# Kernel tuning notes

Measured on AMD Instinct MI355X. Metric: run time of the kernel, lower is better.

The kernel has to match this reference:

```python
import jax, jax.numpy as jnp
import numpy as np

D_MODEL = 1024
NUM_HEADS = 16
HEAD_DIM = D_MODEL // NUM_HEADS
B, S = 2, 2048


def setup_inputs() -> dict:
    key = jax.random.key(0)
    ks = jax.random.split(key, 6)
    scale = 0.02
    return {
        "x": jax.random.normal(ks[0], (B, S, D_MODEL), dtype=jnp.float32),
        "mask": jax.random.normal(ks[1], (S, S), dtype=jnp.float32),
        "Wqkv": jax.random.normal(ks[2], (D_MODEL, 3 * D_MODEL), dtype=jnp.float32) * scale,
        "bqkv": jax.random.normal(ks[3], (3 * D_MODEL,), dtype=jnp.float32) * scale,
        "Wout": jax.random.normal(ks[4], (D_MODEL, D_MODEL), dtype=jnp.float32) * scale,
        "bout": jax.random.normal(ks[5], (D_MODEL,), dtype=jnp.float32) * scale,
    }


def reference(x, mask, Wqkv, bqkv, Wout, bout):
    b, s, d = x.shape
    h, hd = NUM_HEADS, HEAD_DIM
    qkv = x @ Wqkv + bqkv                              # [b, s, 3d]
    qkv = qkv.reshape(b, s, h, 3 * hd).transpose(0, 2, 1, 3)  # [b, h, s, 3hd]
    q, k, v = jnp.split(qkv, 3, axis=-1)               # each [b, h, s, hd]
    scaled = jnp.einsum("bhqd,bhkd->bhqk", q, k) / jnp.sqrt(jnp.float32(hd))
    scaled = scaled + mask                             # mask [s, s] broadcasts
    attn = jax.nn.softmax(scaled, axis=-1)
    values = jnp.einsum("bhqk,bhkd->bhqd", attn, v)    # [b, h, s, hd]
    values = values.transpose(0, 2, 1, 3).reshape(b, s, d)
    return values @ Wout + bout
```

## Files before the change

### kernel.cpp

```cpp
#include <hip/hip_runtime.h>
#include <hip/hip_bf16.h>

#define D_MODEL 1024
#define NH 16
#define HD 64
#define BATCH 2
#define SEQ 2048
#define M_TOTAL (BATCH*SEQ)

typedef _Float16 f16;
typedef _Float16 half8 __attribute__((ext_vector_type(8)));
typedef _Float16 half4v __attribute__((ext_vector_type(4)));
typedef float floatx4 __attribute__((ext_vector_type(4)));

__device__ inline void gload_lds16(const void* g, void* l) {
    __builtin_amdgcn_global_load_lds(
        (const __attribute__((address_space(1))) unsigned int*)g,
        (__attribute__((address_space(3))) unsigned int*)l, 16, 0, 0);
}

__global__ void cvt_f32_f16(const float* __restrict__ src, f16* __restrict__ dst, int n4) {
    int i = blockIdx.x * blockDim.x + threadIdx.x;
    if (i < n4) {
        float4 v = ((const float4*)src)[i];
        half4v o = { (f16)v.x, (f16)v.y, (f16)v.z, (f16)v.w };
        *(half4v*)(dst + (long)i * 4) = o;
    }
}

__global__ void transpose_cvt(const float* __restrict__ src, f16* __restrict__ dst, int R, int C) {
    __shared__ float tile[32][33];
    int tx = threadIdx.x;
    int ty = threadIdx.y;
    int c0 = blockIdx.x * 32;
    int r0 = blockIdx.y * 32;
    for (int yy = 0; yy < 32; yy += 8)
        tile[ty + yy][tx] = src[(long)(r0 + ty + yy) * C + c0 + tx];
    __syncthreads();
    for (int yy = 0; yy < 32; yy += 8)
        dst[(long)(c0 + ty + yy) * R + r0 + tx] = (f16)tile[tx][ty + yy];
}

template<int MODE, int TN>
__global__ __launch_bounds__(256) void gemm_mfma(
    const f16* __restrict__ A, const f16* __restrict__ BT,
    const float* __restrict__ bias,
    f16* __restrict__ Qh, f16* __restrict__ Kh, f16* __restrict__ Vtg,
    float* __restrict__ out, int Kdim)
{
    constexpr int NF = TN / 32;
    __shared__ f16 Ah[128 * 64];
    __shared__ f16 Bh[TN * 64];
    int tid  = threadIdx.x;
    int wid  = tid >> 6;
    int lane = tid & 63;
    int quad = lane >> 4;
    int l16  = lane & 15;
    int m0 = blockIdx.y * 128;
    int n0 = blockIdx.x * TN;
    int mrow = (wid >> 1) * 64;
    int ncol = (wid & 1) * (TN / 2);
    int grow = lane >> 3;
    int gchunk = (lane & 7) ^ (grow & 7);
    int sw0 = ((quad)     ^ (l16 & 7)) * 8;
    int sw1 = ((quad + 4) ^ (l16 & 7)) * 8;

    floatx4 acc[4][NF];
    #pragma unroll
    for (int mb = 0; mb < 4; mb++)
        #pragma unroll
        for (int nb = 0; nb < NF; nb++) acc[mb][nb] = (floatx4){0.f, 0.f, 0.f, 0.f};

    const f16* Abase = A + (long)m0 * Kdim;
    const f16* Bbase = BT + (long)n0 * Kdim;

    for (int k0 = 0; k0 < Kdim; k0 += 64) {
        #pragma unroll
        for (int j = 0; j < 4; j++) {
            int r = j * 32 + wid * 8 + grow;
            gload_lds16(Abase + (long)r * Kdim + k0 + gchunk * 8, &Ah[(j * 32 + wid * 8) * 64]);
        }
        #pragma unroll
        for (int j = 0; j < TN / 32; j++) {
            int r = j * 32 + wid * 8 + grow;
            gload_lds16(Bbase + (long)r * Kdim + k0 + gchunk * 8, &Bh[(j * 32 + wid * 8) * 64]);
        }
        __syncthreads();
        #pragma unroll
        for (int h = 0; h < 2; h++) {
            int sw = h ? sw1 : sw0;
            half8 af[4];
            #pragma unroll
            for (int mb = 0; mb < 4; mb++)
                af[mb] = *(const half8*)&Ah[(mrow + mb * 16 + l16) * 64 + sw];
            #pragma unroll
            for (int nb = 0; nb < NF; nb++) {
                half8 bf = *(const half8*)&Bh[(ncol + nb * 16 + l16) * 64 + sw];
                #pragma unroll
                for (int mb = 0; mb < 4; mb++)
                    acc[mb][nb] = __builtin_amdgcn_mfma_f32_16x16x32_f16(af[mb], bf, acc[mb][nb], 0, 0, 0);
            }
        }
        __syncthreads();
    }

    #pragma unroll
    for (int nb = 0; nb < NF; nb++) {
        int n = n0 + ncol + nb * 16 + l16;
        float bv = bias[n];
        int head = 0, t = 0, d = 0;
        if (MODE == 0) { head = n / 192; int rem = n % 192; t = rem / 64; d = rem % 64; }
        #pragma unroll
        for (int mb = 0; mb < 4; mb++) {
            int mbase = m0 + mrow + mb * 16 + quad * 4;
            if (MODE == 0) {
                int b = mbase >> 11;
                int s = mbase & 2047;
                long bh = b * NH + head;
                if (t == 2) {
                    half4v pack;
                    #pragma unroll
                    for (int r = 0; r < 4; r++) pack[r] = (f16)(acc[mb][nb][r] + bv);
                    *(half4v*)&Vtg[(bh * HD + d) * SEQ + s] = pack;
                } else if (t == 0) {
                    #pragma unroll
                    for (int r = 0; r < 4; r++)
                        Qh[(bh * SEQ + s + r) * HD + d] = (f16)((acc[mb][nb][r] + bv) * 0.125f);
                } else {
                    #pragma unroll
                    for (int r = 0; r < 4; r++)
                        Kh[(bh * SEQ + s + r) * HD + d] = (f16)(acc[mb][nb][r] + bv);
                }
            } else {
                #pragma unroll
                for (int r = 0; r < 4; r++)
                    out[(long)(mbase + r) * D_MODEL + n] = acc[mb][nb][r] + bv;
            }
        }
    }
}

__global__ __launch_bounds__(128) void attn(
    const f16* __restrict__ Qh, const f16* __restrict__ Kh, const f16* __restrict__ Vtg,
    const float* __restrict__ mask, f16* __restrict__ valh)
{
    __shared__ f16 Kl[64 * 64];
    __shared__ f16 Vt[64 * 64];
    __shared__ f16 Pl[2][32 * 72];
    int tid  = threadIdx.x;
    int wid  = tid >> 6;
    int lane = tid & 63;
    int quad = lane >> 4;
    int l16  = lane & 15;
    int bh = blockIdx.y;
    int b  = bh >> 4;
    int h  = bh & 15;
    int q0 = blockIdx.x * 64 + wid * 32;

    int grow8 = lane >> 3;
    int gpos  = lane & 7;
    int sw0 = ((quad)     ^ (l16 & 7)) * 8;
    int sw1 = ((quad + 4) ^ (l16 & 7)) * 8;

    const f16* Qbase = Qh + ((long)bh * SEQ + q0) * HD;
    half8 qf[2][2];
    #pragma unroll
    for (int m = 0; m < 2; m++)
        #pragma unroll
        for (int c = 0; c < 2; c++)
            qf[m][c] = *(const half8*)&Qbase[(long)(m * 16 + l16) * HD + c * 32 + quad * 8];

    half8 vones;
    #pragma unroll
    for (int j = 0; j < 8; j++) vones[j] = (f16)1.0f;

    floatx4 Of[2][4];
    floatx4 Ofs[2];
    #pragma unroll
    for (int m = 0; m < 2; m++) {
        Ofs[m] = (floatx4){0.f, 0.f, 0.f, 0.f};
        #pragma unroll
        for (int nb = 0; nb < 4; nb++) Of[m][nb] = (floatx4){0.f, 0.f, 0.f, 0.f};
    }

    const f16* Kb = Kh + (long)bh * SEQ * HD;
    const f16* Vb = Vtg + (long)bh * HD * SEQ;

    for (int k0 = 0; k0 < SEQ; k0 += 64) {
        __syncthreads();
        #pragma unroll
        for (int j = 0; j < 4; j++) {
            int rb = j * 16 + wid * 8;
            int row = rb + grow8;
            int gk = gpos ^ (row & 7);
            gload_lds16(Kb + (long)(k0 + row) * HD + gk * 8, &Kl[rb * 64]);
            gload_lds16(Vb + (long)row * SEQ + k0 + gk * 8, &Vt[rb * 64]);
        }
        float4 mk[2][4];
        #pragma unroll
        for (int m = 0; m < 2; m++)
            #pragma unroll
            for (int kb = 0; kb < 4; kb++)
                mk[m][kb] = *(const float4*)&mask[(long)(q0 + m * 16 + l16) * SEQ + k0 + kb * 16 + quad * 4];
        __syncthreads();

        #pragma unroll
        for (int kb = 0; kb < 4; kb++) {
            half8 kf0 = *(const half8*)&Kl[(kb * 16 + l16) * 64 + sw0];
            half8 kf1 = *(const half8*)&Kl[(kb * 16 + l16) * 64 + 32 + sw1 - 32];
            #pragma unroll
            for (int m = 0; m < 2; m++) {
                floatx4 s = (floatx4){mk[m][kb].x, mk[m][kb].y, mk[m][kb].z, mk[m][kb].w};
                s = __builtin_amdgcn_mfma_f32_16x16x32_f16(kf0, qf[m][0], s, 0, 0, 0);
                s = __builtin_amdgcn_mfma_f32_16x16x32_f16(kf1, qf[m][1], s, 0, 0, 0);
                half4v ph;
                #pragma unroll
                for (int r = 0; r < 4; r++) ph[r] = (f16)__expf(s[r]);
                *(half4v*)&Pl[wid][(m * 16 + l16) * 72 + kb * 16 + quad * 4] = ph;
            }
        }

        half8 pf[2][2];
        #pragma unroll
        for (int m = 0; m < 2; m++)
            #pragma unroll
            for (int c = 0; c < 2; c++)
                pf[m][c] = *(const half8*)&Pl[wid][(m * 16 + l16) * 72 + c * 32 + quad * 8];

        #pragma unroll
        for (int nb = 0; nb < 4; nb++) {
            half8 vf0 = *(const half8*)&Vt[(nb * 16 + l16) * 64 + sw0];
            half8 vf1 = *(const half8*)&Vt[(nb * 16 + l16) * 64 + sw1];
            #pragma unroll
            for (int m = 0; m < 2; m++) {
                Of[m][nb] = __builtin_amdgcn_mfma_f32_16x16x32_f16(pf[m][0], vf0, Of[m][nb], 0, 0, 0);
                Of[m][nb] = __builtin_amdgcn_mfma_f32_16x16x32_f16(pf[m][1], vf1, Of[m][nb], 0, 0, 0);
            }
        }
        #pragma unroll
        for (int m = 0; m < 2; m++) {
            Ofs[m] = __builtin_amdgcn_mfma_f32_16x16x32_f16(pf[m][0], vones, Ofs[m], 0, 0, 0);
            Ofs[m] = __builtin_amdgcn_mfma_f32_16x16x32_f16(pf[m][1], vones, Ofs[m], 0, 0, 0);
        }
    }

    #pragma unroll
    for (int m = 0; m < 2; m++) {
        floatx4 rs;
        #pragma unroll
        for (int r = 0; r < 4; r++) rs[r] = 1.f / Ofs[m][r];
        #pragma unroll
        for (int nb = 0; nb < 4; nb++)
            #pragma unroll
            for (int r = 0; r < 4; r++) {
                int q = q0 + m * 16 + quad * 4 + r;
                int d = nb * 16 + l16;
                valh[((long)(b * SEQ + q)) * D_MODEL + h * HD + d] = (f16)(Of[m][nb][r] * rs[r]);
            }
    }
}

extern "C" void kernel_launch(void* const* d_in, const int* in_sizes, int n_in,
                              void* d_out, int out_size, void* d_ws, size_t ws_size,
                              hipStream_t stream) {
    const float* x    = (const float*)d_in[0];
    const float* mask = (const float*)d_in[1];
    const float* Wqkv = (const float*)d_in[2];
    const float* bqkv = (const float*)d_in[3];
    const float* Wout = (const float*)d_in[4];
    const float* bout = (const float*)d_in[5];
    float* out = (float*)d_out;

    char* ws = (char*)d_ws;
    f16* xh    = (f16*)(ws + 0);
    f16* WqkvT = (f16*)(ws + 8388608);
    f16* WoutT = (f16*)(ws + 14680064);
    f16* Qh    = (f16*)(ws + 16777216);
    f16* Kh    = (f16*)(ws + 25165824);
    f16* Vtg   = (f16*)(ws + 33554432);
    f16* valh  = (f16*)(ws + 41943040);

    cvt_f32_f16<<<4096, 256, 0, stream>>>(x, xh, M_TOTAL * D_MODEL / 4);
    transpose_cvt<<<dim3(96, 32), dim3(32, 8), 0, stream>>>(Wqkv, WqkvT, 1024, 3072);
    transpose_cvt<<<dim3(32, 32), dim3(32, 8), 0, stream>>>(Wout, WoutT, 1024, 1024);
    gemm_mfma<0, 128><<<dim3(24, 32), 256, 0, stream>>>(xh, WqkvT, bqkv, Qh, Kh, Vtg, nullptr, 1024);
    attn<<<dim3(32, 32), 128, 0, stream>>>(Qh, Kh, Vtg, mask, valh);
    gemm_mfma<1, 64><<<dim3(16, 32), 256, 0, stream>>>(valh, WoutT, bout, nullptr, nullptr, nullptr, out, 1024);
}
```

Before: 258.7 us.

## Precompute exp(mask) in fp16, double-buffer K/V, and widen attention blocks

A new kernel precomputes exp(mask) as fp16 once into reused workspace. The attention kernel then multiplies exp(QK) by it instead of adding the fp32 mask before the exponential, which halves the mask bytes reread for every head. K/V tiles are now double-buffered in LDS with prefetch of the next tile, removing one barrier per iteration. Blocks grow to 4 waves covering 128 query rows, and the P scratch buffer uses an XOR swizzle instead of padding. Risks are an extra kernel launch and a full mask pass, plus fp16 rounding of exp(mask) in the product.

```diff
diff --git a/kernel.cpp b/kernel.cpp
--- a/kernel.cpp
+++ b/kernel.cpp
@@ -24,6 +24,15 @@
     if (i < n4) {
         float4 v = ((const float4*)src)[i];
         half4v o = { (f16)v.x, (f16)v.y, (f16)v.z, (f16)v.w };
+        *(half4v*)(dst + (long)i * 4) = o;
+    }
+}
+
+__global__ void exp_cvt(const float* __restrict__ src, f16* __restrict__ dst, int n4) {
+    int i = blockIdx.x * blockDim.x + threadIdx.x;
+    if (i < n4) {
+        float4 v = ((const float4*)src)[i];
+        half4v o = { (f16)__expf(v.x), (f16)__expf(v.y), (f16)__expf(v.z), (f16)__expf(v.w) };
         *(half4v*)(dst + (long)i * 4) = o;
     }
 }
@@ -140,13 +149,13 @@
     }
 }
 
-__global__ __launch_bounds__(128) void attn(
+__global__ __launch_bounds__(256) void attn(
     const f16* __restrict__ Qh, const f16* __restrict__ Kh, const f16* __restrict__ Vtg,
-    const float* __restrict__ mask, f16* __restrict__ valh)
+    const f16* __restrict__ E, f16* __restrict__ valh)
 {
-    __shared__ f16 Kl[64 * 64];
-    __shared__ f16 Vt[64 * 64];
-    __shared__ f16 Pl[2][32 * 72];
+    __shared__ f16 Kl[2][64 * 64];
+    __shared__ f16 Vt[2][64 * 64];
+    __shared__ f16 Pl[4][32 * 64];
     int tid  = threadIdx.x;
     int wid  = tid >> 6;
     int lane = tid & 63;
@@ -155,10 +164,10 @@
     int bh = blockIdx.y;
     int b  = bh >> 4;
     int h  = bh & 15;
-    int q0 = blockIdx.x * 64 + wid * 32;
-
-    int grow8 = lane >> 3;
-    int gpos  = lane & 7;
+    int q0 = blockIdx.x * 128 + wid * 32;
+
+    int grow = lane >> 3;
+    int gpos = lane & 7;
     int sw0 = ((quad)     ^ (l16 & 7)) * 8;
     int sw1 = ((quad + 4) ^ (l16 & 7)) * 8;
 
@@ -186,37 +195,54 @@
     const f16* Kb = Kh + (long)bh * SEQ * HD;
     const f16* Vb = Vtg + (long)bh * HD * SEQ;
 
-    for (int k0 = 0; k0 < SEQ; k0 += 64) {
+    #pragma unroll
+    for (int j = 0; j < 2; j++) {
+        int rb = j * 32 + wid * 8;
+        int row = rb + grow;
+        int gk = gpos ^ (row & 7);
+        gload_lds16(Kb + (long)row * HD + gk * 8, &Kl[0][rb * 64]);
+        gload_lds16(Vb + (long)row * SEQ + gk * 8, &Vt[0][rb * 64]);
+    }
+
+    for (int it = 0; it < SEQ / 64; it++) {
+        int cur = it & 1;
+        int k0 = it * 64;
         __syncthreads();
-        #pragma unroll
-        for (int j = 0; j < 4; j++) {
-            int rb = j * 16 + wid * 8;
-            int row = rb + grow8;
-            int gk = gpos ^ (row & 7);
-            gload_lds16(Kb + (long)(k0 + row) * HD + gk * 8, &Kl[rb * 64]);
-            gload_lds16(Vb + (long)row * SEQ + k0 + gk * 8, &Vt[rb * 64]);
-        }
-        float4 mk[2][4];
+
+        if (it < SEQ / 64 - 1) {
+            int kn = k0 + 64;
+            #pragma unroll
+            for (int j = 0; j < 2; j++) {
+                int rb = j * 32 + wid * 8;
+                int row = rb + grow;
+                int gk = gpos ^ (row & 7);
+                gload_lds16(Kb + (long)(kn + row) * HD + gk * 8, &Kl[cur ^ 1][rb * 64]);
+                gload_lds16(Vb + (long)row * SEQ + kn + gk * 8, &Vt[cur ^ 1][rb * 64]);
+            }
+        }
+
+        half4v ef[2][4];
         #pragma unroll
         for (int m = 0; m < 2; m++)
             #pragma unroll
             for (int kb = 0; kb < 4; kb++)
-                mk[m][kb] = *(const float4*)&mask[(long)(q0 + m * 16 + l16) * SEQ + k0 + kb * 16 + quad * 4];
-        __syncthreads();
+                ef[m][kb] = *(const half4v*)&E[(long)(q0 + m * 16 + l16) * SEQ + k0 + kb * 16 + quad * 4];
 
         #pragma unroll
         for (int kb = 0; kb < 4; kb++) {
-            half8 kf0 = *(const half8*)&Kl[(kb * 16 + l16) * 64 + sw0];
-            half8 kf1 = *(const half8*)&Kl[(kb * 16 + l16) * 64 + 32 + sw1 - 32];
+            half8 kf0 = *(const half8*)&Kl[cur][(kb * 16 + l16) * 64 + sw0];
+            half8 kf1 = *(const half8*)&Kl[cur][(kb * 16 + l16) * 64 + sw1];
             #pragma unroll
             for (int m = 0; m < 2; m++) {
-                floatx4 s = (floatx4){mk[m][kb].x, mk[m][kb].y, mk[m][kb].z, mk[m][kb].w};
+                floatx4 s = (floatx4){0.f, 0.f, 0.f, 0.f};
                 s = __builtin_amdgcn_mfma_f32_16x16x32_f16(kf0, qf[m][0], s, 0, 0, 0);
                 s = __builtin_amdgcn_mfma_f32_16x16x32_f16(kf1, qf[m][1], s, 0, 0, 0);
                 half4v ph;
                 #pragma unroll
-                for (int r = 0; r < 4; r++) ph[r] = (f16)__expf(s[r]);
-                *(half4v*)&Pl[wid][(m * 16 + l16) * 72 + kb * 16 + quad * 4] = ph;
+                for (int r = 0; r < 4; r++)
+                    ph[r] = (f16)((float)ef[m][kb][r] * __expf(s[r]));
+                int c8 = ((kb * 2 + (quad >> 1)) ^ (l16 & 7)) * 8 + (quad & 1) * 4;
+                *(half4v*)&Pl[wid][(m * 16 + l16) * 64 + c8] = ph;
             }
         }
 
@@ -224,13 +250,15 @@
         #pragma unroll
         for (int m = 0; m < 2; m++)
             #pragma unroll
-            for (int c = 0; c < 2; c++)
-                pf[m][c] = *(const half8*)&Pl[wid][(m * 16 + l16) * 72 + c * 32 + quad * 8];
+            for (int c = 0; c < 2; c++) {
+                int c8 = ((c * 4 + quad) ^ (l16 & 7)) * 8;
+                pf[m][c] = *(const half8*)&Pl[wid][(m * 16 + l16) * 64 + c8];
+            }
 
         #pragma unroll
         for (int nb = 0; nb < 4; nb++) {
-            half8 vf0 = *(const half8*)&Vt[(nb * 16 + l16) * 64 + sw0];
-            half8 vf1 = *(const half8*)&Vt[(nb * 16 + l16) * 64 + sw1];
+            half8 vf0 = *(const half8*)&Vt[cur][(nb * 16 + l16) * 64 + sw0];
+            half8 vf1 = *(const half8*)&Vt[cur][(nb * 16 + l16) * 64 + sw1];
             #pragma unroll
             for (int m = 0; m < 2; m++) {
                 Of[m][nb] = __builtin_amdgcn_mfma_f32_16x16x32_f16(pf[m][0], vf0, Of[m][nb], 0, 0, 0);
@@ -273,6 +301,7 @@
 
     char* ws = (char*)d_ws;
     f16* xh    = (f16*)(ws + 0);
+    f16* E     = (f16*)(ws + 0);
     f16* WqkvT = (f16*)(ws + 8388608);
     f16* WoutT = (f16*)(ws + 14680064);
     f16* Qh    = (f16*)(ws + 16777216);
@@ -284,6 +313,7 @@
     transpose_cvt<<<dim3(96, 32), dim3(32, 8), 0, stream>>>(Wqkv, WqkvT, 1024, 3072);
     transpose_cvt<<<dim3(32, 32), dim3(32, 8), 0, stream>>>(Wout, WoutT, 1024, 1024);
     gemm_mfma<0, 128><<<dim3(24, 32), 256, 0, stream>>>(xh, WqkvT, bqkv, Qh, Kh, Vtg, nullptr, 1024);
-    attn<<<dim3(32, 32), 128, 0, stream>>>(Qh, Kh, Vtg, mask, valh);
+    exp_cvt<<<4096, 256, 0, stream>>>(mask, E, SEQ * SEQ / 4);
+    attn<<<dim3(16, 32), 256, 0, stream>>>(Qh, Kh, Vtg, E, valh);
     gemm_mfma<1, 64><<<dim3(16, 32), 256, 0, stream>>>(valh, WoutT, bout, nullptr, nullptr, nullptr, out, 1024);
 }
```

Result: no change. 259.1 us (+0.1%).
